# Kernel optimization log

Hardware: AMD Instinct MI355X
Metric: run time of the kernel (lower is better)

## Reference

```python
import jax, jax.numpy as jnp
import numpy as np

N_E = 1024
E_DIM = 64
BETA = 0.25


def setup_inputs() -> dict:
    key = jax.random.key(0)
    k1, k2 = jax.random.split(key)
    z = jax.random.normal(k1, (32, 32, 32, E_DIM), dtype=jnp.float32)
    # torch init: uniform(-1/n_e, 1/n_e)
    codebook = jax.random.uniform(k2, (N_E, E_DIM), dtype=jnp.float32,
                                  minval=-1.0 / N_E, maxval=1.0 / N_E)
    return {"z": z, "codebook": codebook}


def reference(z, codebook):
    z_flat = z.reshape(-1, E_DIM)  # [N, e_dim]
    # squared euclidean distances: ||z||^2 + ||e||^2 - 2 z e^T
    d = (jnp.sum(z_flat ** 2, axis=1, keepdims=True)
         + jnp.sum(codebook ** 2, axis=1)
         - 2.0 * jnp.matmul(z_flat, codebook.T))  # [N, n_e]
    idx = jnp.argmin(d, axis=1)  # [N]
    z_q = codebook[idx].reshape(z.shape)
    sg = jax.lax.stop_gradient
    loss = jnp.mean((sg(z_q) - z) ** 2) + BETA * jnp.mean((z_q - sg(z)) ** 2)
    z_q_st = z + sg(z_q - z)  # straight-through estimator
    return z_q_st, idx, loss
```

## Files before the change

### kernel.cpp

```cpp
#include <hip/hip_runtime.h>
#include <hip/hip_bf16.h>

#define NROWS 32768
#define NE    1024
#define ED    64
#define RPB   32
#define RPW   8
#define CHUNK 256

typedef float4 f4;

__global__ __launch_bounds__(256)
void vq_main(const float* __restrict__ z, const float* __restrict__ cb,
             float* __restrict__ out, float* __restrict__ partials)
{
    __shared__ __align__(16) float zsh[RPB * ED];
    __shared__ __align__(16) float et[ED * CHUNK];
    __shared__ __align__(16) float sq[CHUNK];
    __shared__ int   idxsh[RPB];
    __shared__ float wsum[4];

    const int tid  = threadIdx.x;
    const int lane = tid & 63;
    const int w    = tid >> 6;
    const int rowbase = blockIdx.x * RPB;

    {
        const f4* zg = (const f4*)(z + (size_t)rowbase * ED);
        f4* zs = (f4*)zsh;
        zs[tid]       = zg[tid];
        zs[tid + 256] = zg[tid + 256];
    }
    __syncthreads();

    float cn[RPW];
    {
        float rj;
        {
#pragma clang fp contract(off)
            const int rl = lane >> 3;
            const int jj = lane & 7;
            const float* zr = &zsh[(w * RPW + rl) * ED];
            float a = 0.f;
#pragma unroll
            for (int i = 0; i < 8; ++i) { float v = zr[8 * i + jj]; a += v * v; }
            rj = a;
        }
        rj += __shfl_xor(rj, 1);
        rj += __shfl_xor(rj, 2);
        rj += __shfl_xor(rj, 4);
#pragma unroll
        for (int r = 0; r < RPW; ++r) cn[r] = __shfl(rj, r * 8);
    }

    float bestv[RPW];
    int   besti[RPW];
#pragma unroll
    for (int r = 0; r < RPW; ++r) { bestv[r] = INFINITY; besti[r] = 0; }

    const f4* zs4 = (const f4*)zsh;
    const f4* et4 = (const f4*)et;
    const f4* sq4 = (const f4*)sq;

    for (int ch = 0; ch < 4; ++ch) {
        __syncthreads();
        {
            const int code = ch * CHUNK + tid;
            const f4* crow = (const f4*)(cb + (size_t)code * ED);
            float v[ED];
#pragma unroll
            for (int i = 0; i < 16; ++i) {
                f4 t = crow[i];
                v[4 * i + 0] = t.x; v[4 * i + 1] = t.y;
                v[4 * i + 2] = t.z; v[4 * i + 3] = t.w;
            }
            {
#pragma clang fp contract(off)
                float r0 = v[0] * v[0], r1 = v[1] * v[1];
                float r2 = v[2] * v[2], r3 = v[3] * v[3];
                float r4 = v[4] * v[4], r5 = v[5] * v[5];
                float r6 = v[6] * v[6], r7 = v[7] * v[7];
#pragma unroll
                for (int i = 8; i < ED; i += 8) {
                    r0 += v[i + 0] * v[i + 0]; r1 += v[i + 1] * v[i + 1];
                    r2 += v[i + 2] * v[i + 2]; r3 += v[i + 3] * v[i + 3];
                    r4 += v[i + 4] * v[i + 4]; r5 += v[i + 5] * v[i + 5];
                    r6 += v[i + 6] * v[i + 6]; r7 += v[i + 7] * v[i + 7];
                }
                sq[tid] = ((r0 + r1) + (r2 + r3)) + ((r4 + r5) + (r6 + r7));
            }
#pragma unroll
            for (int i = 0; i < ED; ++i) et[i * CHUNK + tid] = v[i];
        }
        __syncthreads();

        f4 sv = sq4[lane];
        float svq[4] = {sv.x, sv.y, sv.z, sv.w};

        float acc[RPW][4];
#pragma unroll
        for (int r = 0; r < RPW; ++r)
            acc[r][0] = acc[r][1] = acc[r][2] = acc[r][3] = 0.f;

#pragma unroll 2
        for (int k4 = 0; k4 < 16; ++k4) {
            f4 e0 = et4[(4 * k4 + 0) * 64 + lane];
            f4 e1 = et4[(4 * k4 + 1) * 64 + lane];
            f4 e2 = et4[(4 * k4 + 2) * 64 + lane];
            f4 e3 = et4[(4 * k4 + 3) * 64 + lane];
#pragma unroll
            for (int r = 0; r < RPW; ++r) {
                f4 zv = zs4[(w * RPW + r) * 16 + k4];
                acc[r][0] = fmaf(zv.x, e0.x, acc[r][0]);
                acc[r][1] = fmaf(zv.x, e0.y, acc[r][1]);
                acc[r][2] = fmaf(zv.x, e0.z, acc[r][2]);
                acc[r][3] = fmaf(zv.x, e0.w, acc[r][3]);
                acc[r][0] = fmaf(zv.y, e1.x, acc[r][0]);
                acc[r][1] = fmaf(zv.y, e1.y, acc[r][1]);
                acc[r][2] = fmaf(zv.y, e1.z, acc[r][2]);
                acc[r][3] = fmaf(zv.y, e1.w, acc[r][3]);
                acc[r][0] = fmaf(zv.z, e2.x, acc[r][0]);
                acc[r][1] = fmaf(zv.z, e2.y, acc[r][1]);
                acc[r][2] = fmaf(zv.z, e2.z, acc[r][2]);
                acc[r][3] = fmaf(zv.z, e2.w, acc[r][3]);
                acc[r][0] = fmaf(zv.w, e3.x, acc[r][0]);
                acc[r][1] = fmaf(zv.w, e3.y, acc[r][1]);
                acc[r][2] = fmaf(zv.w, e3.z, acc[r][2]);
                acc[r][3] = fmaf(zv.w, e3.w, acc[r][3]);
            }
        }

        {
#pragma clang fp contract(off)
#pragma unroll
            for (int r = 0; r < RPW; ++r) {
#pragma unroll
                for (int q = 0; q < 4; ++q) {
                    float t1 = cn[r] + svq[q];
                    float d  = t1 - 2.0f * acc[r][q];
                    int j = ch * 256 + lane * 4 + q;
                    if (d < bestv[r]) { bestv[r] = d; besti[r] = j; }
                }
            }
        }
    }

    float lp = 0.f;
#pragma unroll
    for (int r = 0; r < RPW; ++r) {
        float v = bestv[r];
        int   i = besti[r];
#pragma unroll
        for (int m = 1; m < 64; m <<= 1) {
            float ov = __shfl_xor(v, m);
            int   oi = __shfl_xor(i, m);
            if (ov < v || (ov == v && oi < i)) { v = ov; i = oi; }
        }
        i &= (NE - 1);
        const int grow = rowbase + w * RPW + r;
        float zq, zz, diff, st;
        {
#pragma clang fp contract(off)
            zq   = cb[(size_t)i * ED + lane];
            zz   = zsh[(w * RPW + r) * ED + lane];
            diff = zq - zz;
            st   = zz + diff;
            lp  += diff * diff;
        }
        out[(size_t)grow * ED + lane] = st;
        if (lane == 0) idxsh[w * RPW + r] = i;
    }

#pragma unroll
    for (int m = 1; m < 64; m <<= 1) lp += __shfl_xor(lp, m);
    if (lane == 0) wsum[w] = lp;
    __syncthreads();

    if (tid < RPB) {
        int iv = idxsh[tid] & (NE - 1);
        out[(size_t)NROWS * ED + rowbase + tid] = (float)iv;
    }
    if (tid == 0)
        partials[blockIdx.x] = (wsum[0] + wsum[1]) + (wsum[2] + wsum[3]);
}

__global__ void vq_finalize(const float* __restrict__ partials,
                            float* __restrict__ out)
{
    __shared__ float red[256];
    int t = threadIdx.x;
    float s = (partials[t] + partials[t + 256]) + (partials[t + 512] + partials[t + 768]);
    red[t] = s;
    __syncthreads();
    for (int m = 128; m > 0; m >>= 1) {
        if (t < m) red[t] += red[t + m];
        __syncthreads();
    }
    if (t == 0) {
        float mean = red[0] / (float)((size_t)NROWS * ED);
        float loss = mean + 0.25f * mean;
        out[(size_t)NROWS * ED + NROWS] = loss;
    }
}

extern "C" void kernel_launch(void* const* d_in, const int* in_sizes, int n_in,
                              void* d_out, int out_size, void* d_ws, size_t ws_size,
                              hipStream_t stream)
{
    (void)in_sizes; (void)n_in; (void)out_size; (void)ws_size;
    const float* z  = (const float*)d_in[0];
    const float* cb = (const float*)d_in[1];
    float* out = (float*)d_out;
    float* partials = (float*)d_ws;

    vq_main<<<1024, 256, 0, stream>>>(z, cb, out, partials);
    vq_finalize<<<1, 256, 0, stream>>>(partials, out);
}
```

Before: 90.16 us.

## Restructure VQ kernel: per-thread row in registers, wave-uniform codebook scalar loads

Each thread now keeps one z row in registers. Each wave scans a 128-code slice of the codebook through wave-uniform addresses, which lets the compiler use scalar loads and broadcast values with no LDS staging. The per-wave argmins are then combined through shared memory. Codebook squared norms move into a separate small prep kernel, and the block shape changes to 512 threads covering 64 rows. This removes the LDS transpose and synchronisation, but it adds a kernel launch and heavy register pressure from the 64-float row, and it depends on scalar cache bandwidth for the codebook.

```diff
diff --git a/kernel.cpp b/kernel.cpp
--- a/kernel.cpp
+++ b/kernel.cpp
@@ -1,187 +1,147 @@
 #include <hip/hip_runtime.h>
-#include <hip/hip_bf16.h>
 
 #define NROWS 32768
 #define NE    1024
 #define ED    64
-#define RPB   32
-#define RPW   8
-#define CHUNK 256
 
 typedef float4 f4;
 
-__global__ __launch_bounds__(256)
+__global__ void vq_prep(const float* __restrict__ cb, float* __restrict__ ssq)
+{
+    int j = blockIdx.x * blockDim.x + threadIdx.x;
+    const f4* crow = (const f4*)(cb + (size_t)j * ED);
+    float v[ED];
+#pragma unroll
+    for (int i = 0; i < 16; ++i) {
+        f4 t = crow[i];
+        v[4*i+0] = t.x; v[4*i+1] = t.y; v[4*i+2] = t.z; v[4*i+3] = t.w;
+    }
+    {
+#pragma clang fp contract(off)
+        float r0 = v[0]*v[0], r1 = v[1]*v[1], r2 = v[2]*v[2], r3 = v[3]*v[3];
+        float r4 = v[4]*v[4], r5 = v[5]*v[5], r6 = v[6]*v[6], r7 = v[7]*v[7];
+#pragma unroll
+        for (int i = 8; i < ED; i += 8) {
+            r0 += v[i+0]*v[i+0]; r1 += v[i+1]*v[i+1];
+            r2 += v[i+2]*v[i+2]; r3 += v[i+3]*v[i+3];
+            r4 += v[i+4]*v[i+4]; r5 += v[i+5]*v[i+5];
+            r6 += v[i+6]*v[i+6]; r7 += v[i+7]*v[i+7];
+        }
+        ssq[j] = ((r0+r1)+(r2+r3)) + ((r4+r5)+(r6+r7));
+    }
+}
+
+__global__ __launch_bounds__(512, 4)
 void vq_main(const float* __restrict__ z, const float* __restrict__ cb,
-             float* __restrict__ out, float* __restrict__ partials)
+             const float* __restrict__ ssq, float* __restrict__ out,
+             float* __restrict__ partials)
 {
-    __shared__ __align__(16) float zsh[RPB * ED];
-    __shared__ __align__(16) float et[ED * CHUNK];
-    __shared__ __align__(16) float sq[CHUNK];
-    __shared__ int   idxsh[RPB];
-    __shared__ float wsum[4];
+    __shared__ float cv[8][64];
+    __shared__ int   ci[8][64];
+    __shared__ int   idxsh[64];
+    __shared__ float wsum[8];
 
     const int tid  = threadIdx.x;
     const int lane = tid & 63;
     const int w    = tid >> 6;
-    const int rowbase = blockIdx.x * RPB;
+    const int rowbase = blockIdx.x * 64;
+    const int grow    = rowbase + lane;
 
+    float zr[ED];
     {
-        const f4* zg = (const f4*)(z + (size_t)rowbase * ED);
-        f4* zs = (f4*)zsh;
-        zs[tid]       = zg[tid];
-        zs[tid + 256] = zg[tid + 256];
+        const f4* zrow = (const f4*)(z + (size_t)grow * ED);
+#pragma unroll
+        for (int i = 0; i < 16; ++i) {
+            f4 t = zrow[i];
+            zr[4*i+0] = t.x; zr[4*i+1] = t.y; zr[4*i+2] = t.z; zr[4*i+3] = t.w;
+        }
+    }
+
+    float cn;
+    {
+#pragma clang fp contract(off)
+        float r0 = zr[0]*zr[0], r1 = zr[1]*zr[1], r2 = zr[2]*zr[2], r3 = zr[3]*zr[3];
+        float r4 = zr[4]*zr[4], r5 = zr[5]*zr[5], r6 = zr[6]*zr[6], r7 = zr[7]*zr[7];
+#pragma unroll
+        for (int i = 8; i < ED; i += 8) {
+            r0 += zr[i+0]*zr[i+0]; r1 += zr[i+1]*zr[i+1];
+            r2 += zr[i+2]*zr[i+2]; r3 += zr[i+3]*zr[i+3];
+            r4 += zr[i+4]*zr[i+4]; r5 += zr[i+5]*zr[i+5];
+            r6 += zr[i+6]*zr[i+6]; r7 += zr[i+7]*zr[i+7];
+        }
+        cn = ((r0+r1)+(r2+r3)) + ((r4+r5)+(r6+r7));
+    }
+
+    float bv = INFINITY;
+    int   bi = 0;
+    const int jbase = __builtin_amdgcn_readfirstlane(w * 128);
+
+    for (int jj = 0; jj < 128; jj += 2) {
+        const int j0 = jbase + jj;
+        const float* c0 = cb + (size_t)j0 * ED;
+        float a0 = 0.f, a1 = 0.f;
+#pragma unroll
+        for (int k = 0; k < ED; ++k) {
+            a0 = fmaf(c0[k],      zr[k], a0);
+            a1 = fmaf(c0[ED + k], zr[k], a1);
+        }
+        {
+#pragma clang fp contract(off)
+            float t0 = cn + ssq[j0];
+            float t1 = cn + ssq[j0 + 1];
+            float d0 = t0 - 2.0f * a0;
+            float d1 = t1 - 2.0f * a1;
+            if (d0 < bv) { bv = d0; bi = j0; }
+            if (d1 < bv) { bv = d1; bi = j0 + 1; }
+        }
+    }
+
+    cv[w][lane] = bv;
+    ci[w][lane] = bi;
+    __syncthreads();
+
+    if (tid < 64) {
+        float v = cv[0][tid]; int i = ci[0][tid];
+#pragma unroll
+        for (int u = 1; u < 8; ++u) {
+            float vu = cv[u][tid]; int iu = ci[u][tid];
+            if (vu < v) { v = vu; i = iu; }
+        }
+        i &= (NE - 1);
+        idxsh[tid] = i;
+        out[(size_t)NROWS * ED + rowbase + tid] = (float)i;
     }
     __syncthreads();
 
-    float cn[RPW];
+    const int i = idxsh[lane];
+    const f4* eq  = (const f4*)(cb + (size_t)i * ED + w * 8);
+    const f4* zg2 = (const f4*)(z  + (size_t)grow * ED + w * 8);
+    f4 e0 = eq[0],  e1 = eq[1];
+    f4 z0 = zg2[0], z1 = zg2[1];
+    float lp = 0.f;
+    f4 o0, o1;
     {
-        float rj;
-        {
 #pragma clang fp contract(off)
-            const int rl = lane >> 3;
-            const int jj = lane & 7;
-            const float* zr = &zsh[(w * RPW + rl) * ED];
-            float a = 0.f;
-#pragma unroll
-            for (int i = 0; i < 8; ++i) { float v = zr[8 * i + jj]; a += v * v; }
-            rj = a;
-        }
-        rj += __shfl_xor(rj, 1);
-        rj += __shfl_xor(rj, 2);
-        rj += __shfl_xor(rj, 4);
-#pragma unroll
-        for (int r = 0; r < RPW; ++r) cn[r] = __shfl(rj, r * 8);
+        float d;
+        d = e0.x - z0.x; o0.x = z0.x + d; lp += d*d;
+        d = e0.y - z0.y; o0.y = z0.y + d; lp += d*d;
+        d = e0.z - z0.z; o0.z = z0.z + d; lp += d*d;
+        d = e0.w - z0.w; o0.w = z0.w + d; lp += d*d;
+        d = e1.x - z1.x; o1.x = z1.x + d; lp += d*d;
+        d = e1.y - z1.y; o1.y = z1.y + d; lp += d*d;
+        d = e1.z - z1.z; o1.z = z1.z + d; lp += d*d;
+        d = e1.w - z1.w; o1.w = z1.w + d; lp += d*d;
     }
-
-    float bestv[RPW];
-    int   besti[RPW];
-#pragma unroll
-    for (int r = 0; r < RPW; ++r) { bestv[r] = INFINITY; besti[r] = 0; }
-
-    const f4* zs4 = (const f4*)zsh;
-    const f4* et4 = (const f4*)et;
-    const f4* sq4 = (const f4*)sq;
-
-    for (int ch = 0; ch < 4; ++ch) {
-        __syncthreads();
-        {
-            const int code = ch * CHUNK + tid;
-            const f4* crow = (const f4*)(cb + (size_t)code * ED);
-            float v[ED];
-#pragma unroll
-            for (int i = 0; i < 16; ++i) {
-                f4 t = crow[i];
-                v[4 * i + 0] = t.x; v[4 * i + 1] = t.y;
-                v[4 * i + 2] = t.z; v[4 * i + 3] = t.w;
-            }
-            {
-#pragma clang fp contract(off)
-                float r0 = v[0] * v[0], r1 = v[1] * v[1];
-                float r2 = v[2] * v[2], r3 = v[3] * v[3];
-                float r4 = v[4] * v[4], r5 = v[5] * v[5];
-                float r6 = v[6] * v[6], r7 = v[7] * v[7];
-#pragma unroll
-                for (int i = 8; i < ED; i += 8) {
-                    r0 += v[i + 0] * v[i + 0]; r1 += v[i + 1] * v[i + 1];
-                    r2 += v[i + 2] * v[i + 2]; r3 += v[i + 3] * v[i + 3];
-                    r4 += v[i + 4] * v[i + 4]; r5 += v[i + 5] * v[i + 5];
-                    r6 += v[i + 6] * v[i + 6]; r7 += v[i + 7] * v[i + 7];
-                }
-                sq[tid] = ((r0 + r1) + (r2 + r3)) + ((r4 + r5) + (r6 + r7));
-            }
-#pragma unroll
-            for (int i = 0; i < ED; ++i) et[i * CHUNK + tid] = v[i];
-        }
-        __syncthreads();
-
-        f4 sv = sq4[lane];
-        float svq[4] = {sv.x, sv.y, sv.z, sv.w};
-
-        float acc[RPW][4];
-#pragma unroll
-        for (int r = 0; r < RPW; ++r)
-            acc[r][0] = acc[r][1] = acc[r][2] = acc[r][3] = 0.f;
-
-#pragma unroll 2
-        for (int k4 = 0; k4 < 16; ++k4) {
-            f4 e0 = et4[(4 * k4 + 0) * 64 + lane];
-            f4 e1 = et4[(4 * k4 + 1) * 64 + lane];
-            f4 e2 = et4[(4 * k4 + 2) * 64 + lane];
-            f4 e3 = et4[(4 * k4 + 3) * 64 + lane];
-#pragma unroll
-            for (int r = 0; r < RPW; ++r) {
-                f4 zv = zs4[(w * RPW + r) * 16 + k4];
-                acc[r][0] = fmaf(zv.x, e0.x, acc[r][0]);
-                acc[r][1] = fmaf(zv.x, e0.y, acc[r][1]);
-                acc[r][2] = fmaf(zv.x, e0.z, acc[r][2]);
-                acc[r][3] = fmaf(zv.x, e0.w, acc[r][3]);
-                acc[r][0] = fmaf(zv.y, e1.x, acc[r][0]);
-                acc[r][1] = fmaf(zv.y, e1.y, acc[r][1]);
-                acc[r][2] = fmaf(zv.y, e1.z, acc[r][2]);
-                acc[r][3] = fmaf(zv.y, e1.w, acc[r][3]);
-                acc[r][0] = fmaf(zv.z, e2.x, acc[r][0]);
-                acc[r][1] = fmaf(zv.z, e2.y, acc[r][1]);
-                acc[r][2] = fmaf(zv.z, e2.z, acc[r][2]);
-                acc[r][3] = fmaf(zv.z, e2.w, acc[r][3]);
-                acc[r][0] = fmaf(zv.w, e3.x, acc[r][0]);
-                acc[r][1] = fmaf(zv.w, e3.y, acc[r][1]);
-                acc[r][2] = fmaf(zv.w, e3.z, acc[r][2]);
-                acc[r][3] = fmaf(zv.w, e3.w, acc[r][3]);
-            }
-        }
-
-        {
-#pragma clang fp contract(off)
-#pragma unroll
-            for (int r = 0; r < RPW; ++r) {
-#pragma unroll
-                for (int q = 0; q < 4; ++q) {
-                    float t1 = cn[r] + svq[q];
-                    float d  = t1 - 2.0f * acc[r][q];
-                    int j = ch * 256 + lane * 4 + q;
-                    if (d < bestv[r]) { bestv[r] = d; besti[r] = j; }
-                }
-            }
-        }
-    }
-
-    float lp = 0.f;
-#pragma unroll
-    for (int r = 0; r < RPW; ++r) {
-        float v = bestv[r];
-        int   i = besti[r];
-#pragma unroll
-        for (int m = 1; m < 64; m <<= 1) {
-            float ov = __shfl_xor(v, m);
-            int   oi = __shfl_xor(i, m);
-            if (ov < v || (ov == v && oi < i)) { v = ov; i = oi; }
-        }
-        i &= (NE - 1);
-        const int grow = rowbase + w * RPW + r;
-        float zq, zz, diff, st;
-        {
-#pragma clang fp contract(off)
-            zq   = cb[(size_t)i * ED + lane];
-            zz   = zsh[(w * RPW + r) * ED + lane];
-            diff = zq - zz;
-            st   = zz + diff;
-            lp  += diff * diff;
-        }
-        out[(size_t)grow * ED + lane] = st;
-        if (lane == 0) idxsh[w * RPW + r] = i;
-    }
+    f4* og = (f4*)(out + (size_t)grow * ED + w * 8);
+    og[0] = o0; og[1] = o1;
 
 #pragma unroll
     for (int m = 1; m < 64; m <<= 1) lp += __shfl_xor(lp, m);
     if (lane == 0) wsum[w] = lp;
     __syncthreads();
-
-    if (tid < RPB) {
-        int iv = idxsh[tid] & (NE - 1);
-        out[(size_t)NROWS * ED + rowbase + tid] = (float)iv;
-    }
     if (tid == 0)
-        partials[blockIdx.x] = (wsum[0] + wsum[1]) + (wsum[2] + wsum[3]);
+        partials[blockIdx.x] = (((wsum[0]+wsum[1]) + (wsum[2]+wsum[3]))
+                              + ((wsum[4]+wsum[5]) + (wsum[6]+wsum[7])));
 }
 
 __global__ void vq_finalize(const float* __restrict__ partials,
@@ -189,8 +149,7 @@
 {
     __shared__ float red[256];
     int t = threadIdx.x;
-    float s = (partials[t] + partials[t + 256]) + (partials[t + 512] + partials[t + 768]);
-    red[t] = s;
+    red[t] = partials[t] + partials[t + 256];
     __syncthreads();
     for (int m = 128; m > 0; m >>= 1) {
         if (t < m) red[t] += red[t + m];
@@ -198,8 +157,7 @@
     }
     if (t == 0) {
         float mean = red[0] / (float)((size_t)NROWS * ED);
-        float loss = mean + 0.25f * mean;
-        out[(size_t)NROWS * ED + NROWS] = loss;
+        out[(size_t)NROWS * ED + NROWS] = mean + 0.25f * mean;
     }
 }
 
@@ -211,8 +169,10 @@
     const float* z  = (const float*)d_in[0];
     const float* cb = (const float*)d_in[1];
     float* out = (float*)d_out;
-    float* partials = (float*)d_ws;
+    float* ssq      = (float*)d_ws;
+    float* partials = ssq + NE;
 
-    vq_main<<<1024, 256, 0, stream>>>(z, cb, out, partials);
+    vq_prep<<<4, 256, 0, stream>>>(cb, ssq);
+    vq_main<<<512, 512, 0, stream>>>(z, cb, ssq, out, partials);
     vq_finalize<<<1, 256, 0, stream>>>(partials, out);
 }
```

Result: slower. 97.65 us (+8.3%).
